# Optimization experiments

Measured on AMD Instinct MI355X. Metric: run time of the kernel, lower is better.

The kernel has to match this reference:

```python
import jax, jax.numpy as jnp
import numpy as np

N_NODES = 2048
IN_FEATURES = 1024
N_HEADS = 8
N_HIDDEN = 32  # out_features // n_heads = 256 // 8
NEG_SLOPE = 0.2


def setup_inputs() -> dict:
    key = jax.random.key(0)
    k1, k2, k3, k4 = jax.random.split(key, 4)
    h = jax.random.normal(k1, (N_NODES, IN_FEATURES), dtype=jnp.float32)
    adj_mat = jax.random.randint(k2, (N_NODES, N_NODES, 1), 0, 2).astype(jnp.int32)
    W = jax.random.normal(k3, (IN_FEATURES, N_HEADS * N_HIDDEN), dtype=jnp.float32) * (1.0 / np.sqrt(IN_FEATURES))
    a = jax.random.normal(k4, (2 * N_HIDDEN,), dtype=jnp.float32) * (1.0 / np.sqrt(2 * N_HIDDEN))
    return {"h": h, "adj_mat": adj_mat, "W": W, "a": a}


def reference(h, adj_mat, W, a):
    n = h.shape[0]
    # g: [n, heads, hidden]
    g = (h @ W).reshape(n, N_HEADS, N_HIDDEN)
    # attn Linear on concat([g_i, g_j]) is linear => split weight: e_ij = a_l.g_i + a_r.g_j
    a_l, a_r = a[:N_HIDDEN], a[N_HIDDEN:]
    s_l = jnp.einsum('ihf,f->ih', g, a_l)  # [n, heads]
    s_r = jnp.einsum('jhf,f->jh', g, a_r)  # [n, heads]
    e = s_l[:, None, :] + s_r[None, :, :]  # [n, n, heads]
    e = jnp.where(e >= 0, e, NEG_SLOPE * e)  # leaky relu
    e = jnp.where(adj_mat == 0, -jnp.inf, e)
    att = jax.nn.softmax(e, axis=1)  # softmax over source nodes j
    out = jnp.einsum('ijh,jhf->ihf', att, g)  # [n, heads, hidden]
    return out.reshape(n, N_HEADS * N_HIDDEN)
```

## Files before the change

kernel.cpp:

```cpp
#include <hip/hip_runtime.h>
#include <hip/hip_bf16.h>
#include <math.h>

#define N_NODES 2048
#define IN_F    1024
#define NH      8
#define HF      32
#define OUTF    256
#define LOG2E   1.4426950408889634f

typedef __attribute__((ext_vector_type(8))) short short8;
typedef __attribute__((ext_vector_type(4))) short short4v;
typedef __attribute__((ext_vector_type(4))) float f32x4;

__device__ __forceinline__ short f2bf(float x) {
  unsigned u = __float_as_uint(x);
  return (short)((u + 0x7FFFu + ((u >> 16) & 1u)) >> 16);
}
__device__ __forceinline__ float bf2f(short b) {
  return __uint_as_float(((unsigned)(unsigned short)b) << 16);
}
__device__ __forceinline__ float fexp2(float x) {
#if __has_builtin(__builtin_amdgcn_exp2f)
  return __builtin_amdgcn_exp2f(x);
#else
  return exp2f(x);
#endif
}

__global__ __launch_bounds__(256)
void prep_kernel(const float* __restrict__ h, const int* __restrict__ adj,
                 const float* __restrict__ W, short* __restrict__ h_hi,
                 short* __restrict__ wt_hi, short* __restrict__ wt_lo,
                 unsigned* __restrict__ bits) {
  const int T = blockIdx.x * 256 + threadIdx.x;
  {
    const float4 v0 = *(const float4*)(h + T * 8);
    const float4 v1 = *(const float4*)(h + T * 8 + 4);
    const float x[8] = {v0.x, v0.y, v0.z, v0.w, v1.x, v1.y, v1.z, v1.w};
    short8 hi;
    #pragma unroll
    for (int j = 0; j < 8; ++j) hi[j] = f2bf(x[j]);
    *(short8*)(h_hi + T * 8) = hi;
  }
  if (T < (OUTF * IN_F / 8)) {
    const int kgrp = T >> 8, n = T & 255;
    #pragma unroll
    for (int j = 0; j < 8; ++j) {
      const float x = W[(kgrp * 8 + j) * OUTF + n];
      const short hb = f2bf(x);
      wt_hi[n * IN_F + kgrp * 8 + j] = hb;
      wt_lo[n * IN_F + kgrp * 8 + j] = f2bf(x - bf2f(hb));
    }
  }
  if (T < (N_NODES * 64)) {
    const int4* p = (const int4*)(adj + (T >> 6) * N_NODES + (T & 63) * 32);
    unsigned wbits = 0;
    #pragma unroll
    for (int v = 0; v < 8; ++v) {
      const int4 x = p[v];
      wbits |= (x.x != 0 ? 1u : 0u) << (4 * v + 0);
      wbits |= (x.y != 0 ? 1u : 0u) << (4 * v + 1);
      wbits |= (x.z != 0 ? 1u : 0u) << (4 * v + 2);
      wbits |= (x.w != 0 ? 1u : 0u) << (4 * v + 3);
    }
    bits[T] = wbits;
  }
}

__global__ __launch_bounds__(512)
void gemm_scores_kernel(const short* __restrict__ h_hi,
                        const short* __restrict__ wt_hi, const short* __restrict__ wt_lo,
                        const float* __restrict__ a, short* __restrict__ gt,
                        float* __restrict__ s_l, float* __restrict__ s_r_t) {
  __shared__ float xbuf[4][64][8];
  const int bid = blockIdx.x;
  const int mb = bid >> 2;
  const int nb = bid & 3;
  const int w = threadIdx.x >> 6;
  const int l = threadIdx.x & 63;
  const int il = l & 15, q = l >> 4;
  const int wm = w >> 2;
  const int hp = (w >> 1) & 1;
  const int ks = w & 1;
  const int hh = nb * 2 + hp;
  const int rowb = mb * 32 + wm * 16;
  const int kb = ks * (IN_F / 2);

  const short* ah  = h_hi + (rowb + il) * IN_F + kb;
  const short* bh0 = wt_hi + (hh * HF + il) * IN_F + kb;
  const short* bl0 = wt_lo + (hh * HF + il) * IN_F + kb;
  const short* bh1 = bh0 + 16 * IN_F;
  const short* bl1 = bl0 + 16 * IN_F;

  f32x4 acc0 = {0.f, 0.f, 0.f, 0.f};
  f32x4 acc1 = {0.f, 0.f, 0.f, 0.f};
  #pragma unroll 4
  for (int k0 = 0; k0 < IN_F / 2; k0 += 32) {
    const short8 a_h  = *(const short8*)(ah + k0 + 8 * q);
    const short8 b_h0 = *(const short8*)(bh0 + k0 + 8 * q);
    const short8 b_l0 = *(const short8*)(bl0 + k0 + 8 * q);
    const short8 b_h1 = *(const short8*)(bh1 + k0 + 8 * q);
    const short8 b_l1 = *(const short8*)(bl1 + k0 + 8 * q);
    acc0 = __builtin_amdgcn_mfma_f32_16x16x32_bf16(a_h, b_h0, acc0, 0, 0, 0);
    acc0 = __builtin_amdgcn_mfma_f32_16x16x32_bf16(a_h, b_l0, acc0, 0, 0, 0);
    acc1 = __builtin_amdgcn_mfma_f32_16x16x32_bf16(a_h, b_h1, acc1, 0, 0, 0);
    acc1 = __builtin_amdgcn_mfma_f32_16x16x32_bf16(a_h, b_l1, acc1, 0, 0, 0);
  }

  const int t = w >> 1;
  if (ks == 1) {
    *(f32x4*)&xbuf[t][l][0] = acc0;
    *(f32x4*)&xbuf[t][l][4] = acc1;
  }
  __syncthreads();
  if (ks == 1) return;
  {
    const f32x4 u0 = *(const f32x4*)&xbuf[t][l][0];
    const f32x4 u1 = *(const f32x4*)&xbuf[t][l][4];
    #pragma unroll
    for (int r = 0; r < 4; ++r) { acc0[r] += u0[r]; acc1[r] += u1[r]; }
  }

  {
    short4v p0, p1;
    #pragma unroll
    for (int r = 0; r < 4; ++r) { p0[r] = f2bf(acc0[r]); p1[r] = f2bf(acc1[r]); }
    *(short4v*)(gt + (hh * HF + il) * N_NODES + rowb + 4 * q)      = p0;
    *(short4v*)(gt + (hh * HF + 16 + il) * N_NODES + rowb + 4 * q) = p1;
  }

  const float alv0 = a[il], alv1 = a[16 + il];
  const float arv0 = a[HF + il], arv1 = a[HF + 16 + il];
  float sl[4], sr[4];
  #pragma unroll
  for (int r = 0; r < 4; ++r) {
    sl[r] = acc0[r] * alv0 + acc1[r] * alv1;
    sr[r] = acc0[r] * arv0 + acc1[r] * arv1;
  }
  #pragma unroll
  for (int off = 8; off >= 1; off >>= 1) {
    #pragma unroll
    for (int r = 0; r < 4; ++r) {
      sl[r] += __shfl_xor(sl[r], off, 64);
      sr[r] += __shfl_xor(sr[r], off, 64);
    }
  }
  if (il == 0) {
    #pragma unroll
    for (int r = 0; r < 4; ++r) {
      const int node = rowb + 4 * q + r;
      s_l[node * NH + hh] = sl[r] * LOG2E;
      s_r_t[hh * N_NODES + node] = sr[r] * LOG2E;
    }
  }
}

__global__ __launch_bounds__(512)
void attn_mfma_kernel(const unsigned* __restrict__ bits, const short* __restrict__ gt,
                      const float* __restrict__ s_l, const float* __restrict__ s_r_t,
                      float* __restrict__ out) {
  __shared__ float accbuf[4][64][8];
  __shared__ float dbuf[4][64];
  const int i0 = (blockIdx.x >> 1) * 16;
  const int hg = blockIdx.x & 1;
  const int w  = threadIdx.x >> 6;
  const int l  = threadIdx.x & 63;
  const int hw = w & 3;
  const int js = w >> 2;
  const int hh = hg * 4 + hw;
  const int il = l & 15;
  const int q  = l >> 4;

  const float slv = s_l[(i0 + il) * NH + hh];
  const unsigned* bitrow = bits + (i0 + il) * 64;
  const float* srh = s_r_t + hh * N_NODES;
  const short* g0p = gt + (hh * HF + il) * N_NODES;
  const short* g1p = gt + (hh * HF + 16 + il) * N_NODES;

  f32x4 acc0 = {0.f, 0.f, 0.f, 0.f};
  f32x4 acc1 = {0.f, 0.f, 0.f, 0.f};
  float denom = 0.f;

  const int jbase = js * (N_NODES / 2);
  #pragma unroll 2
  for (int j0 = jbase; j0 < jbase + N_NODES / 2; j0 += 32) {
    const unsigned wq = bitrow[j0 >> 5] >> (8 * q);
    const float4 sra = *(const float4*)(srh + j0 + 8 * q);
    const float4 srb = *(const float4*)(srh + j0 + 8 * q + 4);
    const float sr_[8] = {sra.x, sra.y, sra.z, sra.w, srb.x, srb.y, srb.z, srb.w};
    short8 afrag;
    #pragma unroll
    for (int r = 0; r < 8; ++r) {
      float e = slv + sr_[r];
      e = fmaxf(e, 0.2f * e);
      const float ex = fexp2(e);
      const float wv = ((wq >> r) & 1u) ? ex : 0.f;
      const short wb = f2bf(wv);
      afrag[r] = wb;
      denom += bf2f(wb);
    }
    const short8 b0 = *(const short8*)(g0p + j0 + 8 * q);
    const short8 b1 = *(const short8*)(g1p + j0 + 8 * q);
    acc0 = __builtin_amdgcn_mfma_f32_16x16x32_bf16(afrag, b0, acc0, 0, 0, 0);
    acc1 = __builtin_amdgcn_mfma_f32_16x16x32_bf16(afrag, b1, acc1, 0, 0, 0);
  }

  denom += __shfl_xor(denom, 16, 64);
  denom += __shfl_xor(denom, 32, 64);

  if (js == 1) {
    *(f32x4*)&accbuf[hw][l][0] = acc0;
    *(f32x4*)&accbuf[hw][l][4] = acc1;
    dbuf[hw][l] = denom;
  }
  __syncthreads();
  if (js == 0) {
    const f32x4 u0 = *(const f32x4*)&accbuf[hw][l][0];
    const f32x4 u1 = *(const f32x4*)&accbuf[hw][l][4];
    const float tot = denom + dbuf[hw][l];
    #pragma unroll
    for (int r = 0; r < 4; ++r) {
      const int irow = i0 + 4 * q + r;
      const float inv = 1.0f / __shfl(tot, 4 * q + r, 64);
      out[irow * OUTF + hh * HF + il]      = (acc0[r] + u0[r]) * inv;
      out[irow * OUTF + hh * HF + 16 + il] = (acc1[r] + u1[r]) * inv;
    }
  }
}

extern "C" void kernel_launch(void* const* d_in, const int* in_sizes, int n_in,
                              void* d_out, int out_size, void* d_ws, size_t ws_size,
                              hipStream_t stream) {
  const float* h   = (const float*)d_in[0];
  const int*   adj = (const int*)d_in[1];
  const float* W   = (const float*)d_in[2];
  const float* a   = (const float*)d_in[3];
  float* out = (float*)d_out;

  float* s_l   = (float*)d_ws;
  float* s_r_t = s_l + N_NODES * NH;
  unsigned* bits = (unsigned*)(s_r_t + NH * N_NODES);
  short* gt    = (short*)(bits + N_NODES * 64);
  short* h_hi  = gt + NH * HF * N_NODES;
  short* wt_hi = h_hi + N_NODES * IN_F;
  short* wt_lo = wt_hi + OUTF * IN_F;

  prep_kernel<<<1024, 256, 0, stream>>>(h, adj, W, h_hi, wt_hi, wt_lo, bits);
  gemm_scores_kernel<<<256, 512, 0, stream>>>(h_hi, wt_hi, wt_lo, a, gt, s_l, s_r_t);
  attn_mfma_kernel<<<256, 512, 0, stream>>>(bits, gt, s_l, s_r_t, out);
}
```

Baseline: 56.29 us.

## Split K and J reductions across more waves, one head per block

The GEMM kernel now gives each block a single head and splits K four ways across waves, doubling the grid. The attention kernel assigns one head per block and splits the source-node range eight ways across its waves, reducing the partials through shared memory, so the grid grows from 256 to 1024 blocks. The aim is more parallelism and better occupancy on the many CUs. The cost is extra LDS reduction traffic, a barrier that more waves wait on, and repeated loads of the score and bit rows across blocks.

```diff
diff --git a/kernel.cpp b/kernel.cpp
--- a/kernel.cpp
+++ b/kernel.cpp
@@ -73,19 +73,17 @@
                         const short* __restrict__ wt_hi, const short* __restrict__ wt_lo,
                         const float* __restrict__ a, short* __restrict__ gt,
                         float* __restrict__ s_l, float* __restrict__ s_r_t) {
-  __shared__ float xbuf[4][64][8];
+  __shared__ float xbuf[3][2][64][8];
   const int bid = blockIdx.x;
-  const int mb = bid >> 2;
-  const int nb = bid & 3;
+  const int mb = bid >> 3;
+  const int hh = bid & 7;
   const int w = threadIdx.x >> 6;
   const int l = threadIdx.x & 63;
   const int il = l & 15, q = l >> 4;
   const int wm = w >> 2;
-  const int hp = (w >> 1) & 1;
-  const int ks = w & 1;
-  const int hh = nb * 2 + hp;
+  const int ks = w & 3;
   const int rowb = mb * 32 + wm * 16;
-  const int kb = ks * (IN_F / 2);
+  const int kb = ks * (IN_F / 4);
 
   const short* ah  = h_hi + (rowb + il) * IN_F + kb;
   const short* bh0 = wt_hi + (hh * HF + il) * IN_F + kb;
@@ -96,7 +94,7 @@
   f32x4 acc0 = {0.f, 0.f, 0.f, 0.f};
   f32x4 acc1 = {0.f, 0.f, 0.f, 0.f};
   #pragma unroll 4
-  for (int k0 = 0; k0 < IN_F / 2; k0 += 32) {
+  for (int k0 = 0; k0 < IN_F / 4; k0 += 32) {
     const short8 a_h  = *(const short8*)(ah + k0 + 8 * q);
     const short8 b_h0 = *(const short8*)(bh0 + k0 + 8 * q);
     const short8 b_l0 = *(const short8*)(bl0 + k0 + 8 * q);
@@ -108,16 +106,16 @@
     acc1 = __builtin_amdgcn_mfma_f32_16x16x32_bf16(a_h, b_l1, acc1, 0, 0, 0);
   }
 
-  const int t = w >> 1;
-  if (ks == 1) {
-    *(f32x4*)&xbuf[t][l][0] = acc0;
-    *(f32x4*)&xbuf[t][l][4] = acc1;
+  if (ks) {
+    *(f32x4*)&xbuf[ks - 1][wm][l][0] = acc0;
+    *(f32x4*)&xbuf[ks - 1][wm][l][4] = acc1;
   }
   __syncthreads();
-  if (ks == 1) return;
-  {
-    const f32x4 u0 = *(const f32x4*)&xbuf[t][l][0];
-    const f32x4 u1 = *(const f32x4*)&xbuf[t][l][4];
+  if (ks) return;
+  #pragma unroll
+  for (int s = 0; s < 3; ++s) {
+    const f32x4 u0 = *(const f32x4*)&xbuf[s][wm][l][0];
+    const f32x4 u1 = *(const f32x4*)&xbuf[s][wm][l][4];
     #pragma unroll
     for (int r = 0; r < 4; ++r) { acc0[r] += u0[r]; acc1[r] += u1[r]; }
   }
@@ -160,15 +158,12 @@
 void attn_mfma_kernel(const unsigned* __restrict__ bits, const short* __restrict__ gt,
                       const float* __restrict__ s_l, const float* __restrict__ s_r_t,
                       float* __restrict__ out) {
-  __shared__ float accbuf[4][64][8];
-  __shared__ float dbuf[4][64];
-  const int i0 = (blockIdx.x >> 1) * 16;
-  const int hg = blockIdx.x & 1;
-  const int w  = threadIdx.x >> 6;
+  __shared__ float accbuf[7][64][8];
+  __shared__ float dbuf[7][64];
+  const int i0 = (blockIdx.x >> 3) * 16;
+  const int hh = blockIdx.x & 7;
+  const int js = threadIdx.x >> 6;
   const int l  = threadIdx.x & 63;
-  const int hw = w & 3;
-  const int js = w >> 2;
-  const int hh = hg * 4 + hw;
   const int il = l & 15;
   const int q  = l >> 4;
 
@@ -182,9 +177,9 @@
   f32x4 acc1 = {0.f, 0.f, 0.f, 0.f};
   float denom = 0.f;
 
-  const int jbase = js * (N_NODES / 2);
+  const int jbase = js * (N_NODES / 8);
   #pragma unroll 2
-  for (int j0 = jbase; j0 < jbase + N_NODES / 2; j0 += 32) {
+  for (int j0 = jbase; j0 < jbase + N_NODES / 8; j0 += 32) {
     const unsigned wq = bitrow[j0 >> 5] >> (8 * q);
     const float4 sra = *(const float4*)(srh + j0 + 8 * q);
     const float4 srb = *(const float4*)(srh + j0 + 8 * q + 4);
@@ -209,23 +204,29 @@
   denom += __shfl_xor(denom, 16, 64);
   denom += __shfl_xor(denom, 32, 64);
 
-  if (js == 1) {
-    *(f32x4*)&accbuf[hw][l][0] = acc0;
-    *(f32x4*)&accbuf[hw][l][4] = acc1;
-    dbuf[hw][l] = denom;
+  if (js) {
+    *(f32x4*)&accbuf[js - 1][l][0] = acc0;
+    *(f32x4*)&accbuf[js - 1][l][4] = acc1;
+    dbuf[js - 1][l] = denom;
   }
   __syncthreads();
-  if (js == 0) {
-    const f32x4 u0 = *(const f32x4*)&accbuf[hw][l][0];
-    const f32x4 u1 = *(const f32x4*)&accbuf[hw][l][4];
-    const float tot = denom + dbuf[hw][l];
-    #pragma unroll
-    for (int r = 0; r < 4; ++r) {
-      const int irow = i0 + 4 * q + r;
-      const float inv = 1.0f / __shfl(tot, 4 * q + r, 64);
-      out[irow * OUTF + hh * HF + il]      = (acc0[r] + u0[r]) * inv;
-      out[irow * OUTF + hh * HF + 16 + il] = (acc1[r] + u1[r]) * inv;
-    }
+  if (js) return;
+
+  float tot = denom;
+  #pragma unroll
+  for (int s = 0; s < 7; ++s) {
+    const f32x4 u0 = *(const f32x4*)&accbuf[s][l][0];
+    const f32x4 u1 = *(const f32x4*)&accbuf[s][l][4];
+    #pragma unroll
+    for (int r = 0; r < 4; ++r) { acc0[r] += u0[r]; acc1[r] += u1[r]; }
+    tot += dbuf[s][l];
+  }
+  #pragma unroll
+  for (int r = 0; r < 4; ++r) {
+    const int irow = i0 + 4 * q + r;
+    const float inv = 1.0f / __shfl(tot, 4 * q + r, 64);
+    out[irow * OUTF + hh * HF + il]      = acc0[r] * inv;
+    out[irow * OUTF + hh * HF + 16 + il] = acc1[r] * inv;
   }
 }
 
@@ -247,6 +248,6 @@
   short* wt_lo = wt_hi + OUTF * IN_F;
 
   prep_kernel<<<1024, 256, 0, stream>>>(h, adj, W, h_hi, wt_hi, wt_lo, bits);
-  gemm_scores_kernel<<<256, 512, 0, stream>>>(h_hi, wt_hi, wt_lo, a, gt, s_l, s_r_t);
-  attn_mfma_kernel<<<256, 512, 0, stream>>>(bits, gt, s_l, s_r_t, out);
-}
+  gemm_scores_kernel<<<512, 512, 0, stream>>>(h_hi, wt_hi, wt_lo, a, gt, s_l, s_r_t);
+  attn_mfma_kernel<<<1024, 512, 0, stream>>>(bits, gt, s_l, s_r_t, out);
+}
```

Result: no change. 57.40 us (+2.0%).

## Restructure attention kernel: 32 rows per head per block, 8-way j split

Applied to the files above, without the earlier changes.

Each attention block now handles one head and 32 destination rows, with all 8 waves splitting the source-node range eight ways rather than four heads times two j-halves. Each wave computes two 16-row MFMA tiles, so every loaded g fragment and s_r value is reused across two row tiles, which halves global traffic per unit of work. The grid doubles to 512 blocks. In exchange, registers rise from the extra accumulators, shared memory grows for the 7-way reduction, and wave 0 must serially sum seven partials.

```diff
diff --git a/kernel.cpp b/kernel.cpp
--- a/kernel.cpp
+++ b/kernel.cpp
@@ -160,72 +160,104 @@
 void attn_mfma_kernel(const unsigned* __restrict__ bits, const short* __restrict__ gt,
                       const float* __restrict__ s_l, const float* __restrict__ s_r_t,
                       float* __restrict__ out) {
-  __shared__ float accbuf[4][64][8];
-  __shared__ float dbuf[4][64];
-  const int i0 = (blockIdx.x >> 1) * 16;
-  const int hg = blockIdx.x & 1;
-  const int w  = threadIdx.x >> 6;
+  __shared__ float accbuf[7][64][16];
+  __shared__ float dbuf[7][64][2];
+  const int i0 = (blockIdx.x >> 3) * 32;
+  const int hh = blockIdx.x & 7;
+  const int js = threadIdx.x >> 6;
   const int l  = threadIdx.x & 63;
-  const int hw = w & 3;
-  const int js = w >> 2;
-  const int hh = hg * 4 + hw;
   const int il = l & 15;
   const int q  = l >> 4;
 
-  const float slv = s_l[(i0 + il) * NH + hh];
-  const unsigned* bitrow = bits + (i0 + il) * 64;
+  const float slv0 = s_l[(i0 + il) * NH + hh];
+  const float slv1 = s_l[(i0 + 16 + il) * NH + hh];
+  const unsigned* bitrow0 = bits + (i0 + il) * 64;
+  const unsigned* bitrow1 = bits + (i0 + 16 + il) * 64;
   const float* srh = s_r_t + hh * N_NODES;
   const short* g0p = gt + (hh * HF + il) * N_NODES;
   const short* g1p = gt + (hh * HF + 16 + il) * N_NODES;
 
-  f32x4 acc0 = {0.f, 0.f, 0.f, 0.f};
-  f32x4 acc1 = {0.f, 0.f, 0.f, 0.f};
-  float denom = 0.f;
-
-  const int jbase = js * (N_NODES / 2);
+  f32x4 acc00 = {0.f,0.f,0.f,0.f};
+  f32x4 acc01 = {0.f,0.f,0.f,0.f};
+  f32x4 acc10 = {0.f,0.f,0.f,0.f};
+  f32x4 acc11 = {0.f,0.f,0.f,0.f};
+  float d0 = 0.f, d1 = 0.f;
+
+  const int jbase = js * (N_NODES / 8);
   #pragma unroll 2
-  for (int j0 = jbase; j0 < jbase + N_NODES / 2; j0 += 32) {
-    const unsigned wq = bitrow[j0 >> 5] >> (8 * q);
+  for (int j0 = jbase; j0 < jbase + N_NODES / 8; j0 += 32) {
+    const unsigned wq0 = bitrow0[j0 >> 5] >> (8 * q);
+    const unsigned wq1 = bitrow1[j0 >> 5] >> (8 * q);
     const float4 sra = *(const float4*)(srh + j0 + 8 * q);
     const float4 srb = *(const float4*)(srh + j0 + 8 * q + 4);
     const float sr_[8] = {sra.x, sra.y, sra.z, sra.w, srb.x, srb.y, srb.z, srb.w};
-    short8 afrag;
+    short8 af0, af1;
     #pragma unroll
     for (int r = 0; r < 8; ++r) {
-      float e = slv + sr_[r];
-      e = fmaxf(e, 0.2f * e);
-      const float ex = fexp2(e);
-      const float wv = ((wq >> r) & 1u) ? ex : 0.f;
-      const short wb = f2bf(wv);
-      afrag[r] = wb;
-      denom += bf2f(wb);
+      float e0 = slv0 + sr_[r];
+      e0 = fmaxf(e0, 0.2f * e0);
+      const float w0 = ((wq0 >> r) & 1u) ? fexp2(e0) : 0.f;
+      const short wb0 = f2bf(w0);
+      af0[r] = wb0;
+      d0 += bf2f(wb0);
+      float e1 = slv1 + sr_[r];
+      e1 = fmaxf(e1, 0.2f * e1);
+      const float w1 = ((wq1 >> r) & 1u) ? fexp2(e1) : 0.f;
+      const short wb1 = f2bf(w1);
+      af1[r] = wb1;
+      d1 += bf2f(wb1);
     }
     const short8 b0 = *(const short8*)(g0p + j0 + 8 * q);
     const short8 b1 = *(const short8*)(g1p + j0 + 8 * q);
-    acc0 = __builtin_amdgcn_mfma_f32_16x16x32_bf16(afrag, b0, acc0, 0, 0, 0);
-    acc1 = __builtin_amdgcn_mfma_f32_16x16x32_bf16(afrag, b1, acc1, 0, 0, 0);
-  }
-
-  denom += __shfl_xor(denom, 16, 64);
-  denom += __shfl_xor(denom, 32, 64);
-
-  if (js == 1) {
-    *(f32x4*)&accbuf[hw][l][0] = acc0;
-    *(f32x4*)&accbuf[hw][l][4] = acc1;
-    dbuf[hw][l] = denom;
+    acc00 = __builtin_amdgcn_mfma_f32_16x16x32_bf16(af0, b0, acc00, 0, 0, 0);
+    acc01 = __builtin_amdgcn_mfma_f32_16x16x32_bf16(af0, b1, acc01, 0, 0, 0);
+    acc10 = __builtin_amdgcn_mfma_f32_16x16x32_bf16(af1, b0, acc10, 0, 0, 0);
+    acc11 = __builtin_amdgcn_mfma_f32_16x16x32_bf16(af1, b1, acc11, 0, 0, 0);
+  }
+
+  d0 += __shfl_xor(d0, 16, 64);
+  d0 += __shfl_xor(d0, 32, 64);
+  d1 += __shfl_xor(d1, 16, 64);
+  d1 += __shfl_xor(d1, 32, 64);
+
+  if (js) {
+    float* ab = &accbuf[js - 1][l][0];
+    *(f32x4*)(ab + 0)  = acc00;
+    *(f32x4*)(ab + 4)  = acc01;
+    *(f32x4*)(ab + 8)  = acc10;
+    *(f32x4*)(ab + 12) = acc11;
+    dbuf[js - 1][l][0] = d0;
+    dbuf[js - 1][l][1] = d1;
   }
   __syncthreads();
-  if (js == 0) {
-    const f32x4 u0 = *(const f32x4*)&accbuf[hw][l][0];
-    const f32x4 u1 = *(const f32x4*)&accbuf[hw][l][4];
-    const float tot = denom + dbuf[hw][l];
+  if (js) return;
+
+  float t0 = d0, t1 = d1;
+  #pragma unroll
+  for (int s = 0; s < 7; ++s) {
+    const float* ab = &accbuf[s][l][0];
+    const f32x4 u00 = *(const f32x4*)(ab + 0);
+    const f32x4 u01 = *(const f32x4*)(ab + 4);
+    const f32x4 u10 = *(const f32x4*)(ab + 8);
+    const f32x4 u11 = *(const f32x4*)(ab + 12);
     #pragma unroll
     for (int r = 0; r < 4; ++r) {
-      const int irow = i0 + 4 * q + r;
-      const float inv = 1.0f / __shfl(tot, 4 * q + r, 64);
-      out[irow * OUTF + hh * HF + il]      = (acc0[r] + u0[r]) * inv;
-      out[irow * OUTF + hh * HF + 16 + il] = (acc1[r] + u1[r]) * inv;
-    }
+      acc00[r] += u00[r]; acc01[r] += u01[r];
+      acc10[r] += u10[r]; acc11[r] += u11[r];
+    }
+    t0 += dbuf[s][l][0];
+    t1 += dbuf[s][l][1];
+  }
+  #pragma unroll
+  for (int r = 0; r < 4; ++r) {
+    const int row0 = i0 + 4 * q + r;
+    const int row1 = i0 + 16 + 4 * q + r;
+    const float inv0 = 1.0f / __shfl(t0, 4 * q + r, 64);
+    const float inv1 = 1.0f / __shfl(t1, 4 * q + r, 64);
+    out[row0 * OUTF + hh * HF + il]      = acc00[r] * inv0;
+    out[row0 * OUTF + hh * HF + 16 + il] = acc01[r] * inv0;
+    out[row1 * OUTF + hh * HF + il]      = acc10[r] * inv1;
+    out[row1 * OUTF + hh * HF + 16 + il] = acc11[r] * inv1;
   }
 }
 
@@ -248,5 +280,5 @@
 
   prep_kernel<<<1024, 256, 0, stream>>>(h, adj, W, h_hi, wt_hi, wt_lo, bits);
   gemm_scores_kernel<<<256, 512, 0, stream>>>(h_hi, wt_hi, wt_lo, a, gt, s_l, s_r_t);
-  attn_mfma_kernel<<<256, 512, 0, stream>>>(bits, gt, s_l, s_r_t, out);
-}
+  attn_mfma_kernel<<<512, 512, 0, stream>>>(bits, gt, s_l, s_r_t, out);
+}
```

Result: faster. 50.24 us (-10.7%).
